# Performance work log

Hardware: AMD Instinct MI355X
Metric: run time of the kernel (lower is better)

Reference implementation:

```python
import jax, jax.numpy as jnp
import numpy as np

N, C, HI, WI = 8, 3, 512, 512   # src_img NCHW (input_img_size)
HO, WO = 2048, 2048             # output canvas (output_img_size[2:])
EPS = 1e-8


def _transform_one(img, coor_row):
    """Replicates: sigmoid box params -> theta -> F.affine_grid -> F.grid_sample
    (bilinear, zeros padding, align_corners=False). Theta has zero off-diagonals,
    so the grid is separable in x/y and the bilinear sample factorizes.
    img: [C, HI, WI]; coor_row: [4]. Returns (sample [C,HO,WO], mask [HO,WO])."""
    x = jax.nn.sigmoid(coor_row[0]) * WO
    y = jax.nn.sigmoid(coor_row[1]) * HO
    w = jax.nn.sigmoid(coor_row[2]) * WO
    h = jax.nn.sigmoid(coor_row[3]) * HO
    a = WO / (w + EPS)
    tx = 2.0 / WO * (WO / 2.0 - x) * a
    b = HO / (h + EPS)
    ty = 2.0 / HO * (HO / 2.0 - y) * b
    # affine_grid base coords (align_corners=False): center-of-pixel normalized
    xs = (2.0 * jnp.arange(WO, dtype=img.dtype) + 1.0) / WO - 1.0
    ys = (2.0 * jnp.arange(HO, dtype=img.dtype) + 1.0) / HO - 1.0
    gx = a * xs + tx          # [WO]
    gy = b * ys + ty          # [HO]
    # grid_sample unnormalize (align_corners=False)
    ix = ((gx + 1.0) * WI - 1.0) / 2.0
    iy = ((gy + 1.0) * HI - 1.0) / 2.0
    x0f = jnp.floor(ix); y0f = jnp.floor(iy)
    wx1 = ix - x0f; wx0 = 1.0 - wx1
    wy1 = iy - y0f; wy0 = 1.0 - wy1
    x0 = x0f.astype(jnp.int32); x1 = x0 + 1
    y0 = y0f.astype(jnp.int32); y1 = y0 + 1
    vx0 = ((x0 >= 0) & (x0 < WI)).astype(img.dtype)
    vx1 = ((x1 >= 0) & (x1 < WI)).astype(img.dtype)
    vy0 = ((y0 >= 0) & (y0 < HI)).astype(img.dtype)
    vy1 = ((y1 >= 0) & (y1 < HI)).astype(img.dtype)
    x0c = jnp.clip(x0, 0, WI - 1); x1c = jnp.clip(x1, 0, WI - 1)
    y0c = jnp.clip(y0, 0, HI - 1); y1c = jnp.clip(y1, 0, HI - 1)
    wyv0 = wy0 * vy0; wyv1 = wy1 * vy1
    wxv0 = wx0 * vx0; wxv1 = wx1 * vx1
    # separable bilinear gather with zero padding
    rows = img[:, y0c, :] * wyv0[None, :, None] + img[:, y1c, :] * wyv1[None, :, None]  # [C,HO,WI]
    samp = rows[:, :, x0c] * wxv0[None, None, :] + rows[:, :, x1c] * wxv1[None, None, :]  # [C,HO,WO]
    # grid_sample of an all-ones mask == sum of in-bounds bilinear weights (separable)
    mask = (wyv0 + wyv1)[:, None] * (wxv0 + wxv1)[None, :]  # [HO,WO]
    return samp, mask


def _composite(src_img, bg_img, coor):
    def step(bg, inp):
        img, c = inp
        s, m = _transform_one(img, c)
        bg = bg * (1.0 - m)[None, None] + (s * m[None])[None]
        return bg, None
    bg, _ = jax.lax.scan(step, bg_img, (src_img, coor))
    return bg


def setup_inputs() -> dict:
    key = jax.random.key(0)
    k1, k2, k3 = jax.random.split(key, 3)
    src_img = jax.random.normal(k1, (N, C, HI, WI), dtype=jnp.float32)
    bg_img = jax.random.uniform(k2, (1, C, HO, WO), dtype=jnp.float32)
    coor = jax.random.normal(k3, (N, 4), dtype=jnp.float32)  # nn.Parameter
    return {"src_img": src_img, "bg_img": bg_img, "coor": coor}


def reference(src_img, bg_img, coor):
    return _composite(src_img, bg_img, coor)
```

## Files before the change

kernel.cpp:

```cpp
#include <hip/hip_runtime.h>

#define WI 512
#define HI 512
#define WO 2048
#define HO 2048
#define NIMG 8
#define CCH 3
#define EPS 1e-8f
#define PLANE (HI * WI)

#define TPB   512
#define NWAVE 8
#define WPX   256
#define PXT   4
#define CAPW  520

__launch_bounds__(TPB)
__global__ void diffcomp_v14(const float* __restrict__ src,
                             const float* __restrict__ bg,
                             const float* __restrict__ coor,
                             float* __restrict__ out) {
    __shared__ __align__(16) float cs[NWAVE][CAPW * CCH];
    __shared__ float4 stA[NIMG];
    __shared__ float4 stY[NIMG];

    const int tid = threadIdx.x;
    const int b0  = blockIdx.x;
    const int row = ((b0 & 7) << 8) | (b0 >> 3);
    const float HW1 = 0.5f * (float)(WI - 1);

    if (tid < NIMG) {
        const float cx  = coor[tid * 4 + 0];
        const float cy  = coor[tid * 4 + 1];
        const float cw  = coor[tid * 4 + 2];
        const float chh = coor[tid * 4 + 3];
        const float xx = (1.0f / (1.0f + expf(-cx))) * (float)WO;
        const float yy = (1.0f / (1.0f + expf(-cy))) * (float)HO;
        const float w  = (1.0f / (1.0f + expf(-cw))) * (float)WO;
        const float h  = (1.0f / (1.0f + expf(-chh))) * (float)HO;
        const float a  = (float)WO / (w + EPS);
        const float bb = (float)HO / (h + EPS);
        const float ty = (2.0f / (float)HO) * ((float)HO * 0.5f - yy) * bb;

        const float ys  = (2.0f * (float)row + 1.0f) / (float)HO - 1.0f;
        const float gy  = bb * ys + ty;
        const float iy  = ((gy + 1.0f) * (float)HI - 1.0f) * 0.5f;
        const float y0f = floorf(iy);
        const float fy1 = iy - y0f;
        const float fy0 = 1.0f - fy1;
        const float y1f = y0f + 1.0f;
        const float v0  = (y0f >= 0.0f && y0f < (float)HI) ? 1.0f : 0.0f;
        const float v1  = (y1f >= 0.0f && y1f < (float)HI) ? 1.0f : 0.0f;
        const float wy0 = fy0 * v0;
        const float wy1 = fy1 * v1;
        const float my  = wy0 + wy1;
        const float y0of = fminf(fmaxf(y0f, 0.0f), (float)(HI - 1)) * (float)WI;
        const float y1of = fminf(fmaxf(y1f, 0.0f), (float)(HI - 1)) * (float)WI;

        const float A2 = a * ((float)WI / (float)WO);
        const float D  = 0.5f - xx;

        stA[tid] = make_float4(A2, D, my, wy0);
        stY[tid] = make_float4(wy1, y0of, y1of, 0.0f);
    }
    __syncthreads();

    const int wid  = tid >> 6;
    const int lane = tid & 63;
    const int pw0  = wid << 8;
    const int px0  = pw0 + (lane << 2);
    const int gbase = row * WO + px0;

    unsigned wvis = 0u, wintr = 0u;
    int jw = -1;
#pragma unroll
    for (int n = 0; n < NIMG; n++) {
        const float4 SA = stA[n];
        if (SA.z > 0.0f) {
            const float ixF = fmaf(SA.x, (float)pw0 + SA.y, HW1);
            const float ixL = fmaf(SA.x, (float)(pw0 + WPX - 1) + SA.y, HW1);
            if (!(ixL <= -1.0f || ixF >= (float)WI)) {
                wvis |= (1u << n);
                if (ixF >= 0.0f && ixL < (float)(WI - 1)) {
                    wintr |= (1u << n);
                    if (SA.z == 1.0f) jw = n;
                }
            }
        }
    }
    if (jw >= 0) wvis &= ~((1u << jw) - 1u);

    float acc[CCH][PXT];
    if (jw < 0) {
#pragma unroll
        for (int c = 0; c < CCH; c++) {
            const float4 bv = *(const float4*)&bg[c * (HO * WO) + gbase];
            acc[c][0] = bv.x; acc[c][1] = bv.y; acc[c][2] = bv.z; acc[c][3] = bv.w;
        }
    } else {
#pragma unroll
        for (int c = 0; c < CCH; c++)
#pragma unroll
            for (int p = 0; p < PXT; p++)
                acc[c][p] = 0.0f;
    }

    float xpf[PXT];
#pragma unroll
    for (int p = 0; p < PXT; p++) xpf[p] = (float)(px0 + p);

    float* const slot = cs[wid];

    while (wvis) {
        const int n = (int)__builtin_ctz(wvis);
        wvis &= wvis - 1u;
        const float4 SA = stA[n];
        const float4 SY = stY[n];
        const float A2 = SA.x, Dv = SA.y, my = SA.z;
        const float wy0 = SA.w, wy1 = SY.x;
        const int y0o = (int)SY.y;
        const int y1o = (int)SY.z;

        const float ixF = fmaf(A2, (float)pw0 + Dv, HW1);
        const float ixL = fmaf(A2, (float)(pw0 + WPX - 1) + Dv, HW1);
        const int t0  = (int)fminf(fmaxf(floorf(ixF), 0.0f), (float)(WI - 1));
        const int t1  = (int)fminf(fmaxf(floorf(ixL) + 1.0f, 0.0f), (float)(WI - 1));
        const int t0a = t0 & ~3;
        int R = (t1 - t0a + 4) & ~3;
        if (R > WI - t0a) R = WI - t0a;
        const int lim = t1 - t0a;

        const float* ib = src + n * (CCH * PLANE) + t0a;

#pragma unroll
        for (int sw = 0; sw < 2; sw++) {
            const int xo = (lane << 2) + (sw << 8);
            if (xo < R) {
                float4 r0[CCH], r1[CCH];
#pragma unroll
                for (int c = 0; c < CCH; c++) {
                    r0[c] = *(const float4*)(ib + c * PLANE + y0o + xo);
                    r1[c] = *(const float4*)(ib + c * PLANE + y1o + xo);
                }
                float wv[12];
#pragma unroll
                for (int t = 0; t < 4; t++)
#pragma unroll
                    for (int c = 0; c < CCH; c++)
                        wv[t * CCH + c] = ((const float*)&r0[c])[t] * wy0
                                        + ((const float*)&r1[c])[t] * wy1;
                float* dst = &slot[xo * CCH];
                ((float4*)dst)[0] = make_float4(wv[0], wv[1], wv[2],  wv[3]);
                ((float4*)dst)[1] = make_float4(wv[4], wv[5], wv[6],  wv[7]);
                ((float4*)dst)[2] = make_float4(wv[8], wv[9], wv[10], wv[11]);
            }
        }

        const float t0af = (float)t0a;
        if ((wintr >> n) & 1u) {
            const float omy = 1.0f - my;
            if (omy == 0.0f) {
#pragma unroll
                for (int p = 0; p < PXT; p++) {
                    const float ix  = fmaf(A2, xpf[p] + Dv, HW1);
                    const float x0f = floorf(ix);
                    const float fx1 = ix - x0f;
                    const int   k   = (int)(x0f - t0af);
                    const float* tp = slot + k * CCH;
#pragma unroll
                    for (int c = 0; c < CCH; c++) {
                        const float q0 = tp[c];
                        const float q1 = tp[c + CCH];
                        acc[c][p] = q0 + fx1 * (q1 - q0);
                    }
                }
            } else {
#pragma unroll
                for (int p = 0; p < PXT; p++) {
                    const float ix  = fmaf(A2, xpf[p] + Dv, HW1);
                    const float x0f = floorf(ix);
                    const float fx1 = ix - x0f;
                    const int   k   = (int)(x0f - t0af);
                    const float* tp = slot + k * CCH;
#pragma unroll
                    for (int c = 0; c < CCH; c++) {
                        const float q0 = tp[c];
                        const float q1 = tp[c + CCH];
                        const float sc = q0 + fx1 * (q1 - q0);
                        acc[c][p] = acc[c][p] * omy + my * sc;
                    }
                }
            }
        } else {
#pragma unroll
            for (int p = 0; p < PXT; p++) {
                const float ix  = fmaf(A2, xpf[p] + Dv, HW1);
                const float x0f = floorf(ix);
                const float fx1 = ix - x0f;
                const float fx0 = 1.0f - fx1;
                const float x1f = x0f + 1.0f;
                const float v0  = (x0f >= 0.0f && x0f < (float)WI) ? 1.0f : 0.0f;
                const float v1  = (x1f >= 0.0f && x1f < (float)WI) ? 1.0f : 0.0f;
                const float wx0 = fx0 * v0;
                const float wx1 = fx1 * v1;
                int x0r = (int)fminf(fmaxf(x0f, 0.0f), (float)(WI - 1)) - t0a;
                int x1r = (int)fminf(fmaxf(x1f, 0.0f), (float)(WI - 1)) - t0a;
                x0r = min(max(x0r, 0), lim);
                x1r = min(max(x1r, 0), lim);
                const float m  = my * (wx0 + wx1);
                const float om = 1.0f - m;
#pragma unroll
                for (int c = 0; c < CCH; c++) {
                    const float q0 = slot[x0r * CCH + c];
                    const float q1 = slot[x1r * CCH + c];
                    acc[c][p] = acc[c][p] * om + (q0 * wx0 + q1 * wx1) * m;
                }
            }
        }
    }

#pragma unroll
    for (int c = 0; c < CCH; c++)
        *(float4*)&out[c * (HO * WO) + gbase] =
            make_float4(acc[c][0], acc[c][1], acc[c][2], acc[c][3]);
}

extern "C" void kernel_launch(void* const* d_in, const int* in_sizes, int n_in,
                              void* d_out, int out_size, void* d_ws, size_t ws_size,
                              hipStream_t stream) {
    const float* src  = (const float*)d_in[0];
    const float* bg   = (const float*)d_in[1];
    const float* coor = (const float*)d_in[2];
    float* out = (float*)d_out;
    (void)d_ws; (void)ws_size;

    hipLaunchKernelGGL(diffcomp_v14, dim3(HO), dim3(TPB), 0, stream,
                       src, bg, coor, out);
}
```

Before: 127.5 us.

## Software-pipeline source row loads across visible layers and tighten launch bounds

Builds a list of visible layers and prefetches the first 256-column chunk of the next layer's two source rows into registers while the current layer is blended. This hides global-load latency behind the shared-memory sampling work. The second chunk is still loaded synchronously. It also sets a minimum-blocks hint in launch_bounds, which caps registers and may cause spills now that more registers are needed for prefetch buffers.

```diff
diff --git a/kernel.cpp b/kernel.cpp
--- a/kernel.cpp
+++ b/kernel.cpp
@@ -15,8 +15,8 @@
 #define PXT   4
 #define CAPW  520
 
-__launch_bounds__(TPB)
-__global__ void diffcomp_v14(const float* __restrict__ src,
+__launch_bounds__(TPB, 6)
+__global__ void diffcomp_v15(const float* __restrict__ src,
                              const float* __restrict__ bg,
                              const float* __restrict__ coor,
                              float* __restrict__ out) {
@@ -111,109 +111,152 @@
 
     float* const slot = cs[wid];
 
-    while (wvis) {
-        const int n = (int)__builtin_ctz(wvis);
-        wvis &= wvis - 1u;
-        const float4 SA = stA[n];
-        const float4 SY = stY[n];
-        const float A2 = SA.x, Dv = SA.y, my = SA.z;
-        const float wy0 = SA.w, wy1 = SY.x;
-        const int y0o = (int)SY.y;
-        const int y1o = (int)SY.z;
-
-        const float ixF = fmaf(A2, (float)pw0 + Dv, HW1);
-        const float ixL = fmaf(A2, (float)(pw0 + WPX - 1) + Dv, HW1);
-        const int t0  = (int)fminf(fmaxf(floorf(ixF), 0.0f), (float)(WI - 1));
-        const int t1  = (int)fminf(fmaxf(floorf(ixL) + 1.0f, 0.0f), (float)(WI - 1));
-        const int t0a = t0 & ~3;
-        int R = (t1 - t0a + 4) & ~3;
-        if (R > WI - t0a) R = WI - t0a;
-        const int lim = t1 - t0a;
-
-        const float* ib = src + n * (CCH * PLANE) + t0a;
-
-#pragma unroll
-        for (int sw = 0; sw < 2; sw++) {
-            const int xo = (lane << 2) + (sw << 8);
-            if (xo < R) {
-                float4 r0[CCH], r1[CCH];
+    int lay[NIMG]; int nl = 0;
+    {
+        unsigned t = wvis;
+        while (t) { lay[nl++] = (int)__builtin_ctz(t); t &= t - 1u; }
+    }
+
+    if (nl) {
+        struct LS {
+            float A2, D, my, wy0, wy1;
+            int   t0a, R, lim, y0o, y1o;
+        };
+        LS cur, nxt;
+        float4 PF0[CCH], PF1[CCH];
+
+        auto prefetch = [&](int n, LS& L, float4* r0, float4* r1) {
+            const float4 SA = stA[n];
+            const float4 SY = stY[n];
+            L.A2 = SA.x; L.D = SA.y; L.my = SA.z; L.wy0 = SA.w; L.wy1 = SY.x;
+            L.y0o = (int)SY.y; L.y1o = (int)SY.z;
+            const float ixF = fmaf(L.A2, (float)pw0 + L.D, HW1);
+            const float ixL = fmaf(L.A2, (float)(pw0 + WPX - 1) + L.D, HW1);
+            const int t0 = (int)fminf(fmaxf(floorf(ixF), 0.0f), (float)(WI - 1));
+            const int t1 = (int)fminf(fmaxf(floorf(ixL) + 1.0f, 0.0f), (float)(WI - 1));
+            L.t0a = t0 & ~3;
+            int R = (t1 - L.t0a + 4) & ~3;
+            if (R > WI - L.t0a) R = WI - L.t0a;
+            L.R = R; L.lim = t1 - L.t0a;
+            const int xo = lane << 2;
+            if (xo < L.R) {
+                const float* ib = src + n * (CCH * PLANE) + L.t0a + xo;
 #pragma unroll
                 for (int c = 0; c < CCH; c++) {
-                    r0[c] = *(const float4*)(ib + c * PLANE + y0o + xo);
-                    r1[c] = *(const float4*)(ib + c * PLANE + y1o + xo);
-                }
-                float wv[12];
-#pragma unroll
-                for (int t = 0; t < 4; t++)
-#pragma unroll
-                    for (int c = 0; c < CCH; c++)
-                        wv[t * CCH + c] = ((const float*)&r0[c])[t] * wy0
-                                        + ((const float*)&r1[c])[t] * wy1;
-                float* dst = &slot[xo * CCH];
-                ((float4*)dst)[0] = make_float4(wv[0], wv[1], wv[2],  wv[3]);
-                ((float4*)dst)[1] = make_float4(wv[4], wv[5], wv[6],  wv[7]);
-                ((float4*)dst)[2] = make_float4(wv[8], wv[9], wv[10], wv[11]);
-            }
-        }
-
-        const float t0af = (float)t0a;
-        if ((wintr >> n) & 1u) {
-            const float omy = 1.0f - my;
-            if (omy == 0.0f) {
+                    r0[c] = *(const float4*)(ib + c * PLANE + L.y0o);
+                    r1[c] = *(const float4*)(ib + c * PLANE + L.y1o);
+                }
+            }
+        };
+
+        prefetch(lay[0], nxt, PF0, PF1);
+
+        for (int i = 0; i < nl; i++) {
+            const int n = lay[i];
+            cur = nxt;
+
+            {
+                const int xo = lane << 2;
+                if (xo < cur.R) {
+                    float wv[12];
+#pragma unroll
+                    for (int t = 0; t < 4; t++)
+#pragma unroll
+                        for (int c = 0; c < CCH; c++)
+                            wv[t * CCH + c] = ((const float*)&PF0[c])[t] * cur.wy0
+                                            + ((const float*)&PF1[c])[t] * cur.wy1;
+                    float* dst = &slot[xo * CCH];
+                    ((float4*)dst)[0] = make_float4(wv[0], wv[1], wv[2],  wv[3]);
+                    ((float4*)dst)[1] = make_float4(wv[4], wv[5], wv[6],  wv[7]);
+                    ((float4*)dst)[2] = make_float4(wv[8], wv[9], wv[10], wv[11]);
+                }
+                if (cur.R > 256) {
+                    const int xo1 = (lane << 2) + 256;
+                    if (xo1 < cur.R) {
+                        const float* ib = src + n * (CCH * PLANE) + cur.t0a + xo1;
+                        float4 r0[CCH], r1[CCH];
+#pragma unroll
+                        for (int c = 0; c < CCH; c++) {
+                            r0[c] = *(const float4*)(ib + c * PLANE + cur.y0o);
+                            r1[c] = *(const float4*)(ib + c * PLANE + cur.y1o);
+                        }
+                        float wv[12];
+#pragma unroll
+                        for (int t = 0; t < 4; t++)
+#pragma unroll
+                            for (int c = 0; c < CCH; c++)
+                                wv[t * CCH + c] = ((const float*)&r0[c])[t] * cur.wy0
+                                                + ((const float*)&r1[c])[t] * cur.wy1;
+                        float* dst = &slot[xo1 * CCH];
+                        ((float4*)dst)[0] = make_float4(wv[0], wv[1], wv[2],  wv[3]);
+                        ((float4*)dst)[1] = make_float4(wv[4], wv[5], wv[6],  wv[7]);
+                        ((float4*)dst)[2] = make_float4(wv[8], wv[9], wv[10], wv[11]);
+                    }
+                }
+            }
+
+            if (i + 1 < nl) prefetch(lay[i + 1], nxt, PF0, PF1);
+
+            const float A2 = cur.A2, Dv = cur.D, my = cur.my;
+            const float t0af = (float)cur.t0a;
+            if ((wintr >> n) & 1u) {
+                const float omy = 1.0f - my;
+                if (omy == 0.0f) {
+#pragma unroll
+                    for (int p = 0; p < PXT; p++) {
+                        const float ix  = fmaf(A2, xpf[p] + Dv, HW1);
+                        const float x0f = floorf(ix);
+                        const float fx1 = ix - x0f;
+                        const int   k   = (int)(x0f - t0af);
+                        const float* tp = slot + k * CCH;
+#pragma unroll
+                        for (int c = 0; c < CCH; c++) {
+                            const float q0 = tp[c];
+                            const float q1 = tp[c + CCH];
+                            acc[c][p] = q0 + fx1 * (q1 - q0);
+                        }
+                    }
+                } else {
+#pragma unroll
+                    for (int p = 0; p < PXT; p++) {
+                        const float ix  = fmaf(A2, xpf[p] + Dv, HW1);
+                        const float x0f = floorf(ix);
+                        const float fx1 = ix - x0f;
+                        const int   k   = (int)(x0f - t0af);
+                        const float* tp = slot + k * CCH;
+#pragma unroll
+                        for (int c = 0; c < CCH; c++) {
+                            const float q0 = tp[c];
+                            const float q1 = tp[c + CCH];
+                            const float sc = q0 + fx1 * (q1 - q0);
+                            acc[c][p] = acc[c][p] * omy + my * sc;
+                        }
+                    }
+                }
+            } else {
 #pragma unroll
                 for (int p = 0; p < PXT; p++) {
                     const float ix  = fmaf(A2, xpf[p] + Dv, HW1);
                     const float x0f = floorf(ix);
                     const float fx1 = ix - x0f;
-                    const int   k   = (int)(x0f - t0af);
-                    const float* tp = slot + k * CCH;
+                    const float fx0 = 1.0f - fx1;
+                    const float x1f = x0f + 1.0f;
+                    const float v0  = (x0f >= 0.0f && x0f < (float)WI) ? 1.0f : 0.0f;
+                    const float v1  = (x1f >= 0.0f && x1f < (float)WI) ? 1.0f : 0.0f;
+                    const float wx0 = fx0 * v0;
+                    const float wx1 = fx1 * v1;
+                    int x0r = (int)fminf(fmaxf(x0f, 0.0f), (float)(WI - 1)) - cur.t0a;
+                    int x1r = (int)fminf(fmaxf(x1f, 0.0f), (float)(WI - 1)) - cur.t0a;
+                    x0r = min(max(x0r, 0), cur.lim);
+                    x1r = min(max(x1r, 0), cur.lim);
+                    const float m  = my * (wx0 + wx1);
+                    const float om = 1.0f - m;
 #pragma unroll
                     for (int c = 0; c < CCH; c++) {
-                        const float q0 = tp[c];
-                        const float q1 = tp[c + CCH];
-                        acc[c][p] = q0 + fx1 * (q1 - q0);
-                    }
-                }
-            } else {
-#pragma unroll
-                for (int p = 0; p < PXT; p++) {
-                    const float ix  = fmaf(A2, xpf[p] + Dv, HW1);
-                    const float x0f = floorf(ix);
-                    const float fx1 = ix - x0f;
-                    const int   k   = (int)(x0f - t0af);
-                    const float* tp = slot + k * CCH;
-#pragma unroll
-                    for (int c = 0; c < CCH; c++) {
-                        const float q0 = tp[c];
-                        const float q1 = tp[c + CCH];
-                        const float sc = q0 + fx1 * (q1 - q0);
-                        acc[c][p] = acc[c][p] * omy + my * sc;
-                    }
-                }
-            }
-        } else {
-#pragma unroll
-            for (int p = 0; p < PXT; p++) {
-                const float ix  = fmaf(A2, xpf[p] + Dv, HW1);
-                const float x0f = floorf(ix);
-                const float fx1 = ix - x0f;
-                const float fx0 = 1.0f - fx1;
-                const float x1f = x0f + 1.0f;
-                const float v0  = (x0f >= 0.0f && x0f < (float)WI) ? 1.0f : 0.0f;
-                const float v1  = (x1f >= 0.0f && x1f < (float)WI) ? 1.0f : 0.0f;
-                const float wx0 = fx0 * v0;
-                const float wx1 = fx1 * v1;
-                int x0r = (int)fminf(fmaxf(x0f, 0.0f), (float)(WI - 1)) - t0a;
-                int x1r = (int)fminf(fmaxf(x1f, 0.0f), (float)(WI - 1)) - t0a;
-                x0r = min(max(x0r, 0), lim);
-                x1r = min(max(x1r, 0), lim);
-                const float m  = my * (wx0 + wx1);
-                const float om = 1.0f - m;
-#pragma unroll
-                for (int c = 0; c < CCH; c++) {
-                    const float q0 = slot[x0r * CCH + c];
-                    const float q1 = slot[x1r * CCH + c];
-                    acc[c][p] = acc[c][p] * om + (q0 * wx0 + q1 * wx1) * m;
+                        const float q0 = slot[x0r * CCH + c];
+                        const float q1 = slot[x1r * CCH + c];
+                        acc[c][p] = acc[c][p] * om + (q0 * wx0 + q1 * wx1) * m;
+                    }
                 }
             }
         }
@@ -234,6 +277,6 @@
     float* out = (float*)d_out;
     (void)d_ws; (void)ws_size;
 
-    hipLaunchKernelGGL(diffcomp_v14, dim3(HO), dim3(TPB), 0, stream,
+    hipLaunchKernelGGL(diffcomp_v15, dim3(HO), dim3(TPB), 0, stream,
                        src, bg, coor, out);
 }
```

Measured after the change: 210.2 us. 1.65x slower.
